# Optimization experiments

Measured on AMD Instinct MI355X. Metric: run time of the kernel, lower is better.

Reference implementation:

```python
import jax, jax.numpy as jnp
import numpy as np

B, N, C = 4, 48 * 64, 256
H, W = 48, 64


def _positional_encodings(batch, dtype=jnp.float32):
    # (x^2, y^2, xy, x, y, 1) encoding; matches get_positional_encodings with intrinsics=None
    ys = jnp.linspace(-1.0, 1.0, H, dtype=dtype)
    xs = jnp.linspace(-1.0, 1.0, W, dtype=dtype)
    p3 = jnp.tile(ys, W)            # [N] : ys repeated W times (torch .repeat(B, w))
    p4 = jnp.repeat(xs, H)          # [N] : each x repeated H times (repeat_interleave)
    pos = jnp.stack([p3 * p3, p4 * p4, p3 * p4, p3, p4, jnp.ones_like(p3)], axis=-1)  # [N,6]
    return jnp.broadcast_to(pos, (batch, N, 6))


def setup_inputs() -> dict:
    key = jax.random.key(0)
    k1, k2, k3, k4 = jax.random.split(key, 4)
    x1 = jax.random.normal(k1, (B, N, C), dtype=jnp.float32)
    x2 = jax.random.normal(k2, (B, N, C), dtype=jnp.float32)
    corr = jax.random.normal(k3, (B, 1, H, W, H, W), dtype=jnp.float32)
    W_proj = jax.random.normal(k4, (C + 6, C), dtype=jnp.float32) * (1.0 / np.sqrt(C + 6))
    b_proj = jnp.zeros((C,), dtype=jnp.float32)
    return {"x1": x1, "x2": x2, "corr": corr, "W_proj": W_proj, "b_proj": b_proj}


def reference(x1, x2, corr, W_proj, b_proj):
    b, n, c = x1.shape
    a = corr.reshape(b, n, n)                      # squeeze(1) + double flatten
    # dual softmax (row-wise * column-wise)
    s_row = jax.nn.softmax(a, axis=-1)
    s_col = jax.nn.softmax(a, axis=-2)
    attn_f1 = s_row * s_col                        # [B,N,N]
    attn_f2 = jnp.swapaxes(attn_f1, -2, -1)        # softmax(a^T,-1)*softmax(a^T,-2) == attn_f1^T

    pos = _positional_encodings(b, dtype=x1.dtype)
    v1 = jnp.concatenate([x1, pos], axis=2)        # [B,N,C+6]
    v2 = jnp.concatenate([x2, pos], axis=2)

    # bilinear products v^T @ attn @ v  -> [B, C+6, C+6]
    fund1 = jnp.einsum('bnc,bnm,bmd->bcd', v1, attn_f1, v1)
    fund2 = jnp.einsum('bnc,bnm,bmd->bcd', v2, attn_f2, v2)

    fund1 = jnp.swapaxes(fund1, -2, -1)
    fund2 = jnp.swapaxes(fund2, -2, -1)

    out1 = fund1 @ W_proj + b_proj                 # proj_fundamental
    out2 = fund2 @ W_proj + b_proj
    return (out2, out1)                            # (fundamental_2, fundamental_1)
```

## Files before the change

### kernel.cpp

```cpp
#include <hip/hip_runtime.h>
#include <math.h>

#define NB 4
#define NN 3072
#define NC 256
#define CP 262
#define KG 384
#define XW 528
#define MD 272
#define K3S 4
#define HH 48
#define WW 64
#define LOG2E 1.4426950408889634f

typedef short short8 __attribute__((ext_vector_type(8)));
typedef short short4v __attribute__((ext_vector_type(4)));
typedef float f32x4 __attribute__((ext_vector_type(4)));
typedef unsigned int uint4v __attribute__((ext_vector_type(4)));

__device__ __forceinline__ float fexp2(float x) {
#if __has_builtin(__builtin_amdgcn_exp2f)
    return __builtin_amdgcn_exp2f(x);
#else
    return __exp2f(x);
#endif
}

__device__ __forceinline__ void bsplit(float v, short& h, short& l) {
    unsigned u = __float_as_uint(v);
    h = (short)(u >> 16);
    float r = v - __uint_as_float(u & 0xFFFF0000u);
    l = (short)(__float_as_uint(r) >> 16);
}

__device__ __forceinline__ void fma4(float4& c, float a, float4 b) {
    c.x = fmaf(a, b.x, c.x);
    c.y = fmaf(a, b.y, c.y);
    c.z = fmaf(a, b.z, c.z);
    c.w = fmaf(a, b.w, c.w);
}

__global__ __launch_bounds__(256) void k_stats(const float* __restrict__ corr,
                                               const float* __restrict__ x1,
                                               const float* __restrict__ x2,
                                               float* __restrict__ colpart,
                                               float* __restrict__ rlS,
                                               short* __restrict__ Xh, short* __restrict__ Xl) {
    int bid = blockIdx.x;
    int t = threadIdx.x;
    if (bid < 1024) {
        int chunk = bid & 255;
        int b = bid >> 8;
        int r0 = chunk * 12;
        const float* base = corr + ((size_t)b * NN + r0) * NN;
        f32x4 colacc[3];
        const f32x4 zz = {0.f, 0.f, 0.f, 0.f};
#pragma unroll
        for (int c = 0; c < 3; c++) colacc[c] = zz;
        float rowpart[12];
#pragma unroll 2
        for (int r = 0; r < 12; r++) {
            float rp = 0.f;
#pragma unroll
            for (int cp = 0; cp < 3; cp++) {
                f32x4 v = *(const f32x4*)(base + (size_t)r * NN + cp * 1024 + t * 4);
                f32x4 e;
                e[0] = __expf(v[0]); e[1] = __expf(v[1]);
                e[2] = __expf(v[2]); e[3] = __expf(v[3]);
                colacc[cp] += e;
                rp += (e[0] + e[1]) + (e[2] + e[3]);
            }
            rowpart[r] = rp;
        }
        __shared__ float red[4][12];
        int w = t >> 6, l = t & 63;
#pragma unroll
        for (int r = 0; r < 12; r++) {
            float rp = rowpart[r];
#pragma unroll
            for (int off = 1; off < 64; off <<= 1) rp += __shfl_xor(rp, off);
            if (l == 0) red[w][r] = rp;
        }
        __syncthreads();
        if (t < 12)
            rlS[b * NN + r0 + t] = __log2f(red[0][t] + red[1][t] + red[2][t] + red[3][t]);
        float* cp = colpart + (size_t)(b * 256 + chunk) * NN;
#pragma unroll
        for (int c = 0; c < 3; c++)
            *(f32x4*)(cp + c * 1024 + t * 4) = colacc[c];
    } else {
        int id = (bid - 1024) * 256 + t;
        int col = id % XW;
        int rest = id / XW;
        int kg = rest % KG;
        int b = rest / KG;
        short* ph = Xh + (size_t)id * 8;
        short* pl = Xl + (size_t)id * 8;
        if (col < 512) {
            const float* src = (col < 256 ? x1 : x2) + ((size_t)b * NN + kg * 8) * NC + (col & 255);
#pragma unroll
            for (int j = 0; j < 8; j++) {
                short hs, ls;
                bsplit(src[(size_t)j * NC], hs, ls);
                ph[j] = hs; pl[j] = ls;
            }
        } else {
            int c = col - 512;
#pragma unroll
            for (int j = 0; j < 8; j++) {
                int k = kg * 8 + j;
                int ip4 = k / HH;
                int ip3 = k - ip4 * HH;
                float p3 = -1.f + 2.f * (float)ip3 / 47.f;
                float p4 = -1.f + 2.f * (float)ip4 / 63.f;
                float v = 0.f;
                if (c == 0) v = p3 * p3;
                else if (c == 1) v = p4 * p4;
                else if (c == 2) v = p3 * p4;
                else if (c == 3) v = p3;
                else if (c == 4) v = p4;
                else if (c == 5) v = 1.f;
                short hs, ls;
                bsplit(v, hs, ls);
                ph[j] = hs; pl[j] = ls;
            }
        }
    }
}

__global__ __launch_bounds__(256) void k_comb(const float* __restrict__ colpart,
                                              float* __restrict__ ccS) {
    int bid = blockIdx.x;
    int b = bid / 48, cg = bid - (bid / 48) * 48;
    int t = threadIdx.x;
    int q = t >> 6, c = t & 63;
    int m = cg * 64 + c;
    const float* cp = colpart + (size_t)b * 256 * NN + m;
    float s0 = 0.f, s1 = 0.f, s2 = 0.f, s3 = 0.f;
    int ch0 = q * 64;
    for (int ch = ch0; ch < ch0 + 64; ch += 4) {
        s0 += cp[(size_t)(ch + 0) * NN];
        s1 += cp[(size_t)(ch + 1) * NN];
        s2 += cp[(size_t)(ch + 2) * NN];
        s3 += cp[(size_t)(ch + 3) * NN];
    }
    __shared__ float red[4][64];
    red[q][c] = (s0 + s1) + (s2 + s3);
    __syncthreads();
    if (t < 64)
        ccS[(size_t)b * NN + cg * 64 + t] = __log2f(red[0][t] + red[1][t] + red[2][t] + red[3][t]);
}

struct SMemMain {
    unsigned AH[2][48 * 64];
    unsigned AL[2][48 * 64];
    float ccsh[NN];
};
union SMemU {
    SMemMain m;
    float pdump[4 * 64 * 12];
};

#define LOAD_B4(PH, PL, BHF, BLF)                                            \
    {                                                                        \
        _Pragma("unroll") for (int i_ = 0; i_ < 4; i_++) {                   \
            BHF[i_] = *(const short8*)((PH) + i_ * 128);                     \
            BLF[i_] = *(const short8*)((PL) + i_ * 128);                     \
        }                                                                    \
    }

#define READ_AFRAGS3(BUFH, BUFL, UNIT, AHF, ALF)                             \
    {                                                                        \
        _Pragma("unroll") for (int fr_ = 0; fr_ < 3; fr_++) {                \
            int rowr_ = fr_ * 16 + row16;                                    \
            int uidx_ = rowr_ * 64 + (((UNIT) ^ (rowr_ & 7)) << 2);          \
            AHF[fr_] = *(const short8*)&(BUFH)[uidx_];                       \
            ALF[fr_] = *(const short8*)&(BUFL)[uidx_];                       \
        }                                                                    \
    }

#define MFMA_CLUSTER34(AHF, ALF, BHF, BLF)                                                         \
    {                                                                                              \
        _Pragma("unroll") for (int fr_ = 0; fr_ < 3; fr_++)                                        \
        _Pragma("unroll") for (int i_ = 0; i_ < 4; i_++)                                           \
            acc[fr_][i_] = __builtin_amdgcn_mfma_f32_16x16x32_bf16(AHF[fr_], BHF[i_], acc[fr_][i_], 0, 0, 0); \
        _Pragma("unroll") for (int fr_ = 0; fr_ < 3; fr_++)                                        \
        _Pragma("unroll") for (int i_ = 0; i_ < 4; i_++)                                           \
            acc[fr_][i_] = __builtin_amdgcn_mfma_f32_16x16x32_bf16(AHF[fr_], BLF[i_], acc[fr_][i_], 0, 0, 0); \
        _Pragma("unroll") for (int fr_ = 0; fr_ < 3; fr_++)                                        \
        _Pragma("unroll") for (int i_ = 0; i_ < 4; i_++)                                           \
            acc[fr_][i_] = __builtin_amdgcn_mfma_f32_16x16x32_bf16(ALF[fr_], BHF[i_], acc[fr_][i_], 0, 0, 0); \
    }

#define POS_CLUSTER3(AHF, ALF, PBH, PBL)                                                           \
    {                                                                                              \
        _Pragma("unroll") for (int fr_ = 0; fr_ < 3; fr_++) {                                      \
            accP[fr_] = __builtin_amdgcn_mfma_f32_16x16x32_bf16(AHF[fr_], (PBH), accP[fr_], 0, 0, 0); \
            accP[fr_] = __builtin_amdgcn_mfma_f32_16x16x32_bf16(AHF[fr_], (PBL), accP[fr_], 0, 0, 0); \
            accP[fr_] = __builtin_amdgcn_mfma_f32_16x16x32_bf16(ALF[fr_], (PBH), accP[fr_], 0, 0, 0); \
        }                                                                                          \
    }

#define STAGE_A16(DSTH, DSTL, PC)                                                                 \
    {                                                                                             \
        f32x4 ccv0 = *(const f32x4*)&ccsh[(PC) * 128 + g * 8];                                    \
        f32x4 ccv1 = *(const f32x4*)&ccsh[(PC) * 128 + g * 8 + 4];                                \
        f32x4 ccv2 = *(const f32x4*)&ccsh[(PC) * 128 + 64 + g * 8];                               \
        f32x4 ccv3 = *(const f32x4*)&ccsh[(PC) * 128 + 64 + g * 8 + 4];                           \
        float ev[16];                                                                             \
        _Pragma("unroll") for (int q_ = 0; q_ < 4; q_++) {                                        \
            ev[q_]      = fexp2(fmaf(C2, cr0[q_], rmn) - ccv0[q_]);                               \
            ev[4 + q_]  = fexp2(fmaf(C2, cr1[q_], rmn) - ccv1[q_]);                               \
            ev[8 + q_]  = fexp2(fmaf(C2, cr2[q_], rmn) - ccv2[q_]);                               \
            ev[12 + q_] = fexp2(fmaf(C2, cr3[q_], rmn) - ccv3[q_]);                               \
        }                                                                                         \
        uint4v hi0, hi1, lo0, lo1;                                                                \
        _Pragma("unroll") for (int q_ = 0; q_ < 4; q_++) {                                        \
            unsigned u0 = __float_as_uint(ev[2 * q_]);                                            \
            unsigned u1 = __float_as_uint(ev[2 * q_ + 1]);                                        \
            hi0[q_] = __builtin_amdgcn_perm(u1, u0, 0x07060302u);                                 \
            float r0_ = ev[2 * q_] - __uint_as_float(u0 & 0xffff0000u);                           \
            float r1_ = ev[2 * q_ + 1] - __uint_as_float(u1 & 0xffff0000u);                       \
            lo0[q_] = __builtin_amdgcn_perm(__float_as_uint(r1_), __float_as_uint(r0_), 0x07060302u); \
            unsigned v0 = __float_as_uint(ev[8 + 2 * q_]);                                        \
            unsigned v1 = __float_as_uint(ev[8 + 2 * q_ + 1]);                                    \
            hi1[q_] = __builtin_amdgcn_perm(v1, v0, 0x07060302u);                                 \
            float t0_ = ev[8 + 2 * q_] - __uint_as_float(v0 & 0xffff0000u);                       \
            float t1_ = ev[8 + 2 * q_ + 1] - __uint_as_float(v1 & 0xffff0000u);                   \
            lo1[q_] = __builtin_amdgcn_perm(__float_as_uint(t1_), __float_as_uint(t0_), 0x07060302u); \
        }                                                                                         \
        *(uint4v*)&(DSTH)[widx0] = hi0;                                                           \
        *(uint4v*)&(DSTH)[widx1] = hi1;                                                           \
        *(uint4v*)&(DSTL)[widx0] = lo0;                                                           \
        *(uint4v*)&(DSTL)[widx1] = lo1;                                                           \
    }

__global__ __launch_bounds__(512, 2) void k2_mfma(const float* __restrict__ corr,
        const short* __restrict__ Xh, const short* __restrict__ Xl,
        const float* __restrict__ rlS, const float* __restrict__ ccS,
        short* __restrict__ Zh, short* __restrict__ Zl) {
    __shared__ SMemU sm;
    float* ccsh = sm.m.ccsh;

    const float C2 = 2.f * LOG2E;
    const size_t BSTEP = (size_t)4 * XW * 8;

    int bid = blockIdx.x;
    int xcd = bid & 7, sub = bid >> 3;
    int b = xcd >> 1;
    int rowblk = (xcd & 1) + (sub << 1);
    int n0 = rowblk * 48;

    int t = threadIdx.x;
    int w = t >> 6, l = t & 63;
    int row16 = l & 15, slot = l >> 4;
    bool writer = (t < 384);
    int wrow = t >> 3, g = t & 7;
    int widx0 = wrow * 64 + ((g ^ (wrow & 7)) << 2);
    int widx1 = widx0 + 32;

    {
        const f32x4* src = (const f32x4*)(ccS + (size_t)b * NN);
        for (int i = t; i < NN / 4; i += 512) ((f32x4*)ccsh)[i] = src[i];
    }

    const float* corrR = corr;
    float rmn = 0.f;
    if (writer) {
        corrR = corr + ((size_t)b * NN + n0 + wrow) * NN + g * 8;
        rmn = -rlS[b * NN + n0 + wrow];
    }

    int col0 = w * 64 + row16;
    const short* bh = Xh + ((size_t)(b * KG + slot) * XW + col0) * 8;
    const short* bl = Xl + ((size_t)(b * KG + slot) * XW + col0) * 8;

    f32x4 acc[3][4];
    f32x4 accP[3];
    const f32x4 zz = {0.f, 0.f, 0.f, 0.f};
#pragma unroll
    for (int fr = 0; fr < 3; fr++) {
#pragma unroll
        for (int i = 0; i < 4; i++) acc[fr][i] = zz;
        accP[fr] = zz;
    }

    short8 BhA[4], BlA[4], BhB[4], BlB[4];
    short8 Ph = {0,0,0,0,0,0,0,0}, Pl = Ph;
    LOAD_B4(bh, bl, BhA, BlA);

    f32x4 cr0, cr1, cr2, cr3;
    __syncthreads();
    if (writer) {
        cr0 = *(const f32x4*)(corrR);
        cr1 = *(const f32x4*)(corrR + 4);
        cr2 = *(const f32x4*)(corrR + 64);
        cr3 = *(const f32x4*)(corrR + 68);
        STAGE_A16(sm.m.AH[0], sm.m.AL[0], 0);
        cr0 = *(const f32x4*)(corrR + 128);
        cr1 = *(const f32x4*)(corrR + 132);
        cr2 = *(const f32x4*)(corrR + 192);
        cr3 = *(const f32x4*)(corrR + 196);
    }
    asm volatile("s_waitcnt lgkmcnt(0)" ::: "memory");
    __builtin_amdgcn_s_barrier();

    int cur = 0;
    for (int sp = 0; sp < 24; ++sp) {
        const unsigned* AHc = &sm.m.AH[cur][0];
        const unsigned* ALc = &sm.m.AL[cur][0];
        unsigned* AHn = &sm.m.AH[cur ^ 1][0];
        unsigned* ALn = &sm.m.AL[cur ^ 1][0];
        short8 Ah[3], Al[3];
        if (w < 4) {
            size_t o0 = ((size_t)(b * KG + sp * 16 + 4 * w + slot) * XW + 512 + row16) * 8;
            Ph = *(const short8*)(Xh + o0);
            Pl = *(const short8*)(Xl + o0);
        }
        READ_AFRAGS3(AHc, ALc, slot, Ah, Al);
        bh += BSTEP; bl += BSTEP;
        LOAD_B4(bh, bl, BhB, BlB);
        __builtin_amdgcn_s_setprio(1);
        MFMA_CLUSTER34(Ah, Al, BhA, BlA);
        if (w == 0) POS_CLUSTER3(Ah, Al, Ph, Pl);
        __builtin_amdgcn_s_setprio(0);
        READ_AFRAGS3(AHc, ALc, 4 + slot, Ah, Al);
        bh += BSTEP; bl += BSTEP;
        LOAD_B4(bh, bl, BhA, BlA);
        __builtin_amdgcn_s_setprio(1);
        MFMA_CLUSTER34(Ah, Al, BhB, BlB);
        if (w == 1) POS_CLUSTER3(Ah, Al, Ph, Pl);
        __builtin_amdgcn_s_setprio(0);
        if (writer) {
            int pc = (sp + 1 < 24) ? sp + 1 : 23;
            STAGE_A16(AHn, ALn, pc);
        }
        READ_AFRAGS3(AHc, ALc, 8 + slot, Ah, Al);
        bh += BSTEP; bl += BSTEP;
        LOAD_B4(bh, bl, BhB, BlB);
        __builtin_amdgcn_s_setprio(1);
        MFMA_CLUSTER34(Ah, Al, BhA, BlA);
        if (w == 2) POS_CLUSTER3(Ah, Al, Ph, Pl);
        __builtin_amdgcn_s_setprio(0);
        if (writer) {
            int pn = (sp + 2 < 24) ? sp + 2 : 23;
            cr0 = *(const f32x4*)(corrR + pn * 128);
            cr1 = *(const f32x4*)(corrR + pn * 128 + 4);
            cr2 = *(const f32x4*)(corrR + pn * 128 + 64);
            cr3 = *(const f32x4*)(corrR + pn * 128 + 68);
        }
        READ_AFRAGS3(AHc, ALc, 12 + slot, Ah, Al);
        if (sp < 23) {
            bh += BSTEP; bl += BSTEP;
            LOAD_B4(bh, bl, BhA, BlA);
        }
        __builtin_amdgcn_s_setprio(1);
        MFMA_CLUSTER34(Ah, Al, BhB, BlB);
        if (w == 3) POS_CLUSTER3(Ah, Al, Ph, Pl);
        __builtin_amdgcn_s_setprio(0);
        asm volatile("s_waitcnt lgkmcnt(0)" ::: "memory");
        __builtin_amdgcn_s_barrier();
        cur ^= 1;
    }

#pragma unroll
    for (int fr = 0; fr < 3; fr++) {
        int kgz = rowblk * 6 + fr * 2 + (slot >> 1);
        int jb = (slot & 1) << 2;
#pragma unroll
        for (int i = 0; i < 4; i++) {
            int colv = w * 64 + i * 16 + row16;
            size_t off = ((size_t)(b * KG + kgz) * XW + colv) * 8 + jb;
            short4v zh, zl;
#pragma unroll
            for (int r = 0; r < 4; r++) {
                short hs, ls; bsplit(acc[fr][i][r], hs, ls);
                zh[r] = hs; zl[r] = ls;
            }
            *(short4v*)(Zh + off) = zh;
            *(short4v*)(Zl + off) = zl;
        }
    }
    if (w < 4) {
#pragma unroll
        for (int fr = 0; fr < 3; fr++)
            *(f32x4*)&sm.pdump[(size_t)(w * 64 + l) * 12 + fr * 4] = accP[fr];
    }
    __syncthreads();
    if (t < 192) {
        int fr = t >> 6, ll = t & 63;
        int sl = ll >> 4, r16 = ll & 15;
        f32x4 s = zz;
#pragma unroll
        for (int ww = 0; ww < 4; ww++)
            s += *(const f32x4*)&sm.pdump[(size_t)(ww * 64 + ll) * 12 + fr * 4];
        int kgz = rowblk * 6 + fr * 2 + (sl >> 1);
        int jb = (sl & 1) << 2;
        size_t off = ((size_t)(b * KG + kgz) * XW + 512 + r16) * 8 + jb;
        short4v zh, zl;
#pragma unroll
        for (int r = 0; r < 4; r++) {
            short hs, ls; bsplit(s[r], hs, ls);
            zh[r] = hs; zl[r] = ls;
        }
        *(short4v*)(Zh + off) = zh;
        *(short4v*)(Zl + off) = zl;
    }
}

__global__ __launch_bounds__(256) void k3_mfma(const short* __restrict__ Xh, const short* __restrict__ Xl,
                                               const short* __restrict__ Zh, const short* __restrict__ Zl,
                                               float* __restrict__ Mpart) {
    int tile = blockIdx.x;
    int rt = tile / 3, ct = tile % 3;
    int mb = blockIdx.y;
    int mat = mb >> 2, b = mb & 3;
    int split = blockIdx.z;

    const int O0[4] = {0, 6, 12, 17};
    int r0f = O0[rt], rNf = O0[rt + 1] - r0f;
    int c0f = O0[ct], cNf = O0[ct + 1] - c0f;

    int t = threadIdx.x;
    int w = t >> 6, l = t & 63;
    int row16 = l & 15, slot = l >> 4;
    int wr = w >> 1, wc = w & 1;
    int rh = (rNf + 1) >> 1;
    int rbeg = r0f + (wr ? rh : 0);
    int rcnt = wr ? (rNf - rh) : rh;
    int chh = (cNf + 1) >> 1;
    int cbeg = c0f + (wc ? chh : 0);
    int ccnt = wc ? (cNf - chh) : chh;

    const short *Ah_, *Al_, *Bh_, *Bl_;
    int abase, bbase;
    if (mat == 0) { Ah_ = Xh; Al_ = Xl; Bh_ = Zh; Bl_ = Zl; abase = 0; bbase = 0; }
    else          { Ah_ = Zh; Al_ = Zl; Bh_ = Xh; Bl_ = Xl; abase = 256; bbase = 256; }

    int acol[3], bcol[3];
#pragma unroll
    for (int i = 0; i < 3; i++) {
        int fa = rbeg + i;
        acol[i] = ((fa < 16) ? (abase + fa * 16) : 512) + row16;
        int fb = cbeg + i;
        bcol[i] = ((fb < 16) ? (bbase + fb * 16) : 512) + row16;
    }

    f32x4 acc[3][3];
    const f32x4 zz = {0.f, 0.f, 0.f, 0.f};
#pragma unroll
    for (int i = 0; i < 3; i++)
#pragma unroll
        for (int j = 0; j < 3; j++) acc[i][j] = zz;

    for (int it = 0; it < 24; it++) {
        int kg = split * 96 + it * 4 + slot;
        size_t base = (size_t)(b * KG + kg) * XW;
        short8 Ah[3], Al[3], Bhf[3], Blf[3];
#pragma unroll
        for (int i = 0; i < 3; i++) {
            if (i < rcnt) {
                Ah[i] = *(const short8*)(Ah_ + (base + acol[i]) * 8);
                Al[i] = *(const short8*)(Al_ + (base + acol[i]) * 8);
            }
            if (i < ccnt) {
                Bhf[i] = *(const short8*)(Bh_ + (base + bcol[i]) * 8);
                Blf[i] = *(const short8*)(Bl_ + (base + bcol[i]) * 8);
            }
        }
#pragma unroll
        for (int i = 0; i < 3; i++) {
            if (i < rcnt) {
#pragma unroll
                for (int j = 0; j < 3; j++) {
                    if (j < ccnt) {
                        acc[i][j] = __builtin_amdgcn_mfma_f32_16x16x32_bf16(Ah[i], Bhf[j], acc[i][j], 0, 0, 0);
                        acc[i][j] = __builtin_amdgcn_mfma_f32_16x16x32_bf16(Al[i], Bhf[j], acc[i][j], 0, 0, 0);
                        acc[i][j] = __builtin_amdgcn_mfma_f32_16x16x32_bf16(Ah[i], Blf[j], acc[i][j], 0, 0, 0);
                    }
                }
            }
        }
    }

    float* Mp = Mpart + (size_t)(mb * K3S + split) * (MD * MD);
#pragma unroll
    for (int i = 0; i < 3; i++) {
        if (i < rcnt) {
#pragma unroll
            for (int j = 0; j < 3; j++) {
                if (j < ccnt) {
                    int r = (rbeg + i) * 16 + slot * 4;
                    int c = (cbeg + j) * 16 + row16;
#pragma unroll
                    for (int q = 0; q < 4; q++)
                        Mp[(size_t)(r + q) * MD + c] = acc[i][j][q];
                }
            }
        }
    }
}

__global__ __launch_bounds__(256) void k_mcombine(const float* __restrict__ Mpart, float* __restrict__ M) {
    const int per = MD * MD;
    int f4 = blockIdx.x * 256 + threadIdx.x;
    if (f4 >= (8 * per) / 4) return;
    int e = f4 * 4;
    int mb = e / per;
    int off = e - mb * per;
    const float* src = Mpart + (size_t)mb * K3S * per + off;
    float4 s = make_float4(0.f, 0.f, 0.f, 0.f);
#pragma unroll
    for (int sp = 0; sp < K3S; sp++) {
        float4 v = *(const float4*)(src + (size_t)sp * per);
        s.x += v.x; s.y += v.y; s.z += v.z; s.w += v.w;
    }
    *(float4*)(M + (size_t)mb * per + off) = s;
}

__global__ __launch_bounds__(256) void k4_proj(const float* __restrict__ M, const float* __restrict__ Wp,
                                               const float* __restrict__ bp, float* __restrict__ out) {
    int i0 = blockIdx.x * 16;
    int b = blockIdx.y;
    int mat = blockIdx.z;
    const float* Mp = M + (size_t)(mat * 4 + b) * (MD * MD);
    int t = threadIdx.x;
    int jt = t & 63, it = t >> 6;
    int j = jt * 4;
    float4 a0 = make_float4(0.f, 0.f, 0.f, 0.f), a1 = a0, a2 = a0, a3 = a0;
#pragma unroll 2
    for (int k = 0; k < CP; k++) {
        float4 w = *(const float4*)(Wp + (size_t)k * NC + j);
        float4 g = *(const float4*)(Mp + (size_t)k * MD + i0 + it * 4);
        fma4(a0, g.x, w); fma4(a1, g.y, w); fma4(a2, g.z, w); fma4(a3, g.w, w);
    }
    float4 bb = *(const float4*)(bp + j);
    a0.x += bb.x; a0.y += bb.y; a0.z += bb.z; a0.w += bb.w;
    a1.x += bb.x; a1.y += bb.y; a1.z += bb.z; a1.w += bb.w;
    a2.x += bb.x; a2.y += bb.y; a2.z += bb.z; a2.w += bb.w;
    a3.x += bb.x; a3.y += bb.y; a3.z += bb.z; a3.w += bb.w;
    float* ob = out + (mat == 0 ? (size_t)NB * CP * NC : (size_t)0) + (size_t)b * CP * NC;
    int i = i0 + it * 4;
    if (i + 0 < CP) *(float4*)(ob + (size_t)(i + 0) * NC + j) = a0;
    if (i + 1 < CP) *(float4*)(ob + (size_t)(i + 1) * NC + j) = a1;
    if (i + 2 < CP) *(float4*)(ob + (size_t)(i + 2) * NC + j) = a2;
    if (i + 3 < CP) *(float4*)(ob + (size_t)(i + 3) * NC + j) = a3;
}

extern "C" void kernel_launch(void* const* d_in, const int* in_sizes, int n_in,
                              void* d_out, int out_size, void* d_ws, size_t ws_size,
                              hipStream_t stream) {
    const float* x1 = (const float*)d_in[0];
    const float* x2 = (const float*)d_in[1];
    const float* corr = (const float*)d_in[2];
    const float* Wp = (const float*)d_in[3];
    const float* bp = (const float*)d_in[4];
    float* out = (float*)d_out;
    float* w = (float*)d_ws;

    const size_t XSZ = (size_t)NB * KG * XW * 8;

    size_t o = 0;
    float* rlS = w + o;     o += NB * NN;
    float* ccS = w + o;     o += NB * NN;
    float* colpart = w + o; o += (size_t)NB * 256 * NN;
    short* Xh = (short*)(w + o); o += XSZ / 2;
    short* Xl = (short*)(w + o); o += XSZ / 2;
    short* Zh = (short*)(w + o); o += XSZ / 2;
    short* Zl = (short*)(w + o); o += XSZ / 2;
    float* Mpart = w + o; o += (size_t)8 * K3S * MD * MD;
    float* M = w + o;     o += (size_t)8 * MD * MD;

    k_stats<<<dim3(4192), dim3(256), 0, stream>>>(corr, x1, x2, colpart, rlS, Xh, Xl);
    k_comb<<<dim3(192), dim3(256), 0, stream>>>(colpart, ccS);
    k2_mfma<<<dim3(256), dim3(512), 0, stream>>>(corr, Xh, Xl, rlS, ccS, Zh, Zl);
    k3_mfma<<<dim3(9, 8, K3S), dim3(256), 0, stream>>>(Xh, Xl, Zh, Zl, Mpart);
    k_mcombine<<<dim3(578), dim3(256), 0, stream>>>(Mpart, M);
    k4_proj<<<dim3(17, NB, 2), dim3(256), 0, stream>>>(M, Wp, bp, out);
}
```

Before: 267.4 us.

## Split k2 reduction over two K halves and add a Z partial-sum combine kernel

k2_mfma now splits its 3072-long reduction into two halves, doubling its grid to 512 blocks, and raises launch bounds to 4 blocks per CU. Each half writes its own partial Z buffer, and a new k_zadd kernel sums the two hi/lo bf16 partials and re-splits the result. k3 moves to 8 K-splits with half the iterations each, and the workspace layout is rearranged so colpart aliases Mpart. The goal is more parallelism and occupancy in the dominant kernel. In exchange it adds an extra kernel launch, extra Z memory traffic, and a risk of register spills under the tighter launch bound.

```diff
diff --git a/kernel.cpp b/kernel.cpp
--- a/kernel.cpp
+++ b/kernel.cpp
@@ -8,10 +8,11 @@
 #define KG 384
 #define XW 528
 #define MD 272
-#define K3S 4
+#define K3S 8
 #define HH 48
 #define WW 64
 #define LOG2E 1.4426950408889634f
+#define XSZ_S ((size_t)NB * KG * XW * 8)
 
 typedef short short8 __attribute__((ext_vector_type(8)));
 typedef short short4v __attribute__((ext_vector_type(4)));
@@ -203,10 +204,10 @@
 
 #define STAGE_A16(DSTH, DSTL, PC)                                                                 \
     {                                                                                             \
-        f32x4 ccv0 = *(const f32x4*)&ccsh[(PC) * 128 + g * 8];                                    \
-        f32x4 ccv1 = *(const f32x4*)&ccsh[(PC) * 128 + g * 8 + 4];                                \
-        f32x4 ccv2 = *(const f32x4*)&ccsh[(PC) * 128 + 64 + g * 8];                               \
-        f32x4 ccv3 = *(const f32x4*)&ccsh[(PC) * 128 + 64 + g * 8 + 4];                           \
+        f32x4 ccv0 = *(const f32x4*)&ccb[(PC) * 128 + g * 8];                                     \
+        f32x4 ccv1 = *(const f32x4*)&ccb[(PC) * 128 + g * 8 + 4];                                 \
+        f32x4 ccv2 = *(const f32x4*)&ccb[(PC) * 128 + 64 + g * 8];                                \
+        f32x4 ccv3 = *(const f32x4*)&ccb[(PC) * 128 + 64 + g * 8 + 4];                            \
         float ev[16];                                                                             \
         _Pragma("unroll") for (int q_ = 0; q_ < 4; q_++) {                                        \
             ev[q_]      = fexp2(fmaf(C2, cr0[q_], rmn) - ccv0[q_]);                               \
@@ -235,7 +236,7 @@
         *(uint4v*)&(DSTL)[widx1] = lo1;                                                           \
     }
 
-__global__ __launch_bounds__(512, 2) void k2_mfma(const float* __restrict__ corr,
+__global__ __launch_bounds__(512, 4) void k2_mfma(const float* __restrict__ corr,
         const short* __restrict__ Xh, const short* __restrict__ Xl,
         const float* __restrict__ rlS, const float* __restrict__ ccS,
         short* __restrict__ Zh, short* __restrict__ Zl) {
@@ -248,8 +249,11 @@
     int bid = blockIdx.x;
     int xcd = bid & 7, sub = bid >> 3;
     int b = xcd >> 1;
-    int rowblk = (xcd & 1) + (sub << 1);
+    int split = sub >> 5;
+    int subr = sub & 31;
+    int rowblk = (xcd & 1) + (subr << 1);
     int n0 = rowblk * 48;
+    int koff = split * 1536;
 
     int t = threadIdx.x;
     int w = t >> 6, l = t & 63;
@@ -263,17 +267,18 @@
         const f32x4* src = (const f32x4*)(ccS + (size_t)b * NN);
         for (int i = t; i < NN / 4; i += 512) ((f32x4*)ccsh)[i] = src[i];
     }
+    const float* ccb = ccsh + koff;
 
     const float* corrR = corr;
     float rmn = 0.f;
     if (writer) {
-        corrR = corr + ((size_t)b * NN + n0 + wrow) * NN + g * 8;
+        corrR = corr + ((size_t)b * NN + n0 + wrow) * NN + koff + g * 8;
         rmn = -rlS[b * NN + n0 + wrow];
     }
 
     int col0 = w * 64 + row16;
-    const short* bh = Xh + ((size_t)(b * KG + slot) * XW + col0) * 8;
-    const short* bl = Xl + ((size_t)(b * KG + slot) * XW + col0) * 8;
+    const short* bh = Xh + ((size_t)(b * KG + split * 192 + slot) * XW + col0) * 8;
+    const short* bl = Xl + ((size_t)(b * KG + split * 192 + slot) * XW + col0) * 8;
 
     f32x4 acc[3][4];
     f32x4 accP[3];
@@ -306,14 +311,14 @@
     __builtin_amdgcn_s_barrier();
 
     int cur = 0;
-    for (int sp = 0; sp < 24; ++sp) {
+    for (int sp = 0; sp < 12; ++sp) {
         const unsigned* AHc = &sm.m.AH[cur][0];
         const unsigned* ALc = &sm.m.AL[cur][0];
         unsigned* AHn = &sm.m.AH[cur ^ 1][0];
         unsigned* ALn = &sm.m.AL[cur ^ 1][0];
         short8 Ah[3], Al[3];
         if (w < 4) {
-            size_t o0 = ((size_t)(b * KG + sp * 16 + 4 * w + slot) * XW + 512 + row16) * 8;
+            size_t o0 = ((size_t)(b * KG + split * 192 + sp * 16 + 4 * w + slot) * XW + 512 + row16) * 8;
             Ph = *(const short8*)(Xh + o0);
             Pl = *(const short8*)(Xl + o0);
         }
@@ -332,7 +337,7 @@
         if (w == 1) POS_CLUSTER3(Ah, Al, Ph, Pl);
         __builtin_amdgcn_s_setprio(0);
         if (writer) {
-            int pc = (sp + 1 < 24) ? sp + 1 : 23;
+            int pc = (sp + 1 < 12) ? sp + 1 : 11;
             STAGE_A16(AHn, ALn, pc);
         }
         READ_AFRAGS3(AHc, ALc, 8 + slot, Ah, Al);
@@ -343,14 +348,14 @@
         if (w == 2) POS_CLUSTER3(Ah, Al, Ph, Pl);
         __builtin_amdgcn_s_setprio(0);
         if (writer) {
-            int pn = (sp + 2 < 24) ? sp + 2 : 23;
+            int pn = (sp + 2 < 12) ? sp + 2 : 11;
             cr0 = *(const f32x4*)(corrR + pn * 128);
             cr1 = *(const f32x4*)(corrR + pn * 128 + 4);
             cr2 = *(const f32x4*)(corrR + pn * 128 + 64);
             cr3 = *(const f32x4*)(corrR + pn * 128 + 68);
         }
         READ_AFRAGS3(AHc, ALc, 12 + slot, Ah, Al);
-        if (sp < 23) {
+        if (sp < 11) {
             bh += BSTEP; bl += BSTEP;
             LOAD_B4(bh, bl, BhA, BlA);
         }
@@ -363,6 +368,8 @@
         cur ^= 1;
     }
 
+    short* Zho = Zh + (size_t)split * XSZ_S;
+    short* Zlo = Zl + (size_t)split * XSZ_S;
 #pragma unroll
     for (int fr = 0; fr < 3; fr++) {
         int kgz = rowblk * 6 + fr * 2 + (slot >> 1);
@@ -377,8 +384,8 @@
                 short hs, ls; bsplit(acc[fr][i][r], hs, ls);
                 zh[r] = hs; zl[r] = ls;
             }
-            *(short4v*)(Zh + off) = zh;
-            *(short4v*)(Zl + off) = zl;
+            *(short4v*)(Zho + off) = zh;
+            *(short4v*)(Zlo + off) = zl;
         }
     }
     if (w < 4) {
@@ -403,9 +410,31 @@
             short hs, ls; bsplit(s[r], hs, ls);
             zh[r] = hs; zl[r] = ls;
         }
-        *(short4v*)(Zh + off) = zh;
-        *(short4v*)(Zl + off) = zl;
-    }
+        *(short4v*)(Zho + off) = zh;
+        *(short4v*)(Zlo + off) = zl;
+    }
+}
+
+__global__ __launch_bounds__(256) void k_zadd(short* __restrict__ Zh, short* __restrict__ Zl) {
+    size_t id = (size_t)blockIdx.x * 256 + threadIdx.x;
+    size_t off = id * 8;
+    short8 ha = *(const short8*)(Zh + off);
+    short8 hb = *(const short8*)(Zh + XSZ_S + off);
+    short8 la = *(const short8*)(Zl + off);
+    short8 lb = *(const short8*)(Zl + XSZ_S + off);
+    short8 oh, ol;
+#pragma unroll
+    for (int j = 0; j < 8; j++) {
+        float va = __uint_as_float((unsigned)(unsigned short)ha[j] << 16)
+                 + __uint_as_float((unsigned)(unsigned short)la[j] << 16);
+        float vb = __uint_as_float((unsigned)(unsigned short)hb[j] << 16)
+                 + __uint_as_float((unsigned)(unsigned short)lb[j] << 16);
+        short hs, ls;
+        bsplit(va + vb, hs, ls);
+        oh[j] = hs; ol[j] = ls;
+    }
+    *(short8*)(Zh + off) = oh;
+    *(short8*)(Zl + off) = ol;
 }
 
 __global__ __launch_bounds__(256) void k3_mfma(const short* __restrict__ Xh, const short* __restrict__ Xl,
@@ -453,8 +482,8 @@
 #pragma unroll
         for (int j = 0; j < 3; j++) acc[i][j] = zz;
 
-    for (int it = 0; it < 24; it++) {
-        int kg = split * 96 + it * 4 + slot;
+    for (int it = 0; it < 12; it++) {
+        int kg = split * 48 + it * 4 + slot;
         size_t base = (size_t)(b * KG + kg) * XW;
         short8 Ah[3], Al[3], Bhf[3], Blf[3];
 #pragma unroll
@@ -558,22 +587,21 @@
     float* out = (float*)d_out;
     float* w = (float*)d_ws;
 
-    const size_t XSZ = (size_t)NB * KG * XW * 8;
-
     size_t o = 0;
     float* rlS = w + o;     o += NB * NN;
     float* ccS = w + o;     o += NB * NN;
-    float* colpart = w + o; o += (size_t)NB * 256 * NN;
-    short* Xh = (short*)(w + o); o += XSZ / 2;
-    short* Xl = (short*)(w + o); o += XSZ / 2;
-    short* Zh = (short*)(w + o); o += XSZ / 2;
-    short* Zl = (short*)(w + o); o += XSZ / 2;
-    float* Mpart = w + o; o += (size_t)8 * K3S * MD * MD;
-    float* M = w + o;     o += (size_t)8 * MD * MD;
+    float* colpart = w + o;
+    float* Mpart = w + o;   o += (size_t)8 * K3S * MD * MD;
+    float* M = w + o;       o += (size_t)8 * MD * MD;
+    short* Xh = (short*)(w + o); o += XSZ_S / 2;
+    short* Xl = (short*)(w + o); o += XSZ_S / 2;
+    short* Zh = (short*)(w + o); o += XSZ_S;
+    short* Zl = (short*)(w + o); o += XSZ_S;
 
     k_stats<<<dim3(4192), dim3(256), 0, stream>>>(corr, x1, x2, colpart, rlS, Xh, Xl);
     k_comb<<<dim3(192), dim3(256), 0, stream>>>(colpart, ccS);
-    k2_mfma<<<dim3(256), dim3(512), 0, stream>>>(corr, Xh, Xl, rlS, ccS, Zh, Zl);
+    k2_mfma<<<dim3(512), dim3(512), 0, stream>>>(corr, Xh, Xl, rlS, ccS, Zh, Zl);
+    k_zadd<<<dim3(3168), dim3(256), 0, stream>>>(Zh, Zl);
     k3_mfma<<<dim3(9, 8, K3S), dim3(256), 0, stream>>>(Xh, Xl, Zh, Zl, Mpart);
     k_mcombine<<<dim3(578), dim3(256), 0, stream>>>(Mpart, M);
     k4_proj<<<dim3(17, NB, 2), dim3(256), 0, stream>>>(M, Wp, bp, out);
```

New measurement: 665.4 us. +148.9%, slower.
